# Performance work log

Measured on AMD Instinct MI355X. Metric: run time of the kernel, lower is better.

The kernel has to match this reference:

```python
import jax, jax.numpy as jnp
import numpy as np

B, T, D, H, L, F = 256, 32, 1024, 8, 3, 2048
SSRC, NCOL, NTAB, NACT, NSYM = 64, 32, 16, 64, 32
HD = D // H


def setup_inputs() -> dict:
    key = jax.random.key(0)
    ks = jax.random.split(key, 40)
    n = lambda k, s, sc=0.02: jax.random.normal(k, s, jnp.float32) * sc
    inp = {}
    inp["prev_action_emb"] = jax.random.normal(ks[0], (B, T, D), jnp.float32)
    inp["encoded_src"] = jax.random.normal(ks[1], (B, SSRC, D), jnp.float32)
    inp["encoded_col"] = jax.random.normal(ks[2], (B, NCOL, D), jnp.float32)
    inp["encoded_tab"] = jax.random.normal(ks[3], (B, NTAB, D), jnp.float32)
    inp["src_mask"] = jnp.zeros((B, SSRC), jnp.int32)  # 1 = padded
    inp["symbol_ids"] = jax.random.randint(ks[4], (B, T), 0, NSYM)
    inp["view_type"] = jax.random.randint(ks[5], (B,), 0, 3)  # 0=action,1=col,2=tab
    inp["gold_action"] = jax.random.randint(ks[6], (B,), 0, NACT)
    inp["gold_col"] = jax.random.randint(ks[7], (B,), 0, NCOL)
    inp["gold_tab"] = jax.random.randint(ks[8], (B,), 0, NTAB)
    # grammar embeddings (torch nn.Embedding default ~ N(0,1))
    inp["symbol_emb"] = jax.random.normal(ks[9], (NSYM, D), jnp.float32)
    inp["action_emb"] = jax.random.normal(ks[10], (NACT, D), jnp.float32)
    # affine heads
    inp["action_aff_w"] = n(ks[11], (D, D)); inp["action_aff_b"] = jnp.zeros((D,), jnp.float32)
    inp["symbol_aff_w"] = n(ks[12], (D, D)); inp["symbol_aff_b"] = jnp.zeros((D,), jnp.float32)
    inp["col_aff_w"] = n(ks[13], (D, D)); inp["col_aff_b"] = jnp.zeros((D,), jnp.float32)
    inp["tab_aff_w"] = n(ks[14], (D, D)); inp["tab_aff_b"] = jnp.zeros((D,), jnp.float32)
    inp["tgt_lin_w"] = n(ks[15], (2 * D, D)); inp["tgt_lin_b"] = jnp.zeros((D,), jnp.float32)
    inp["out_lin_w"] = n(ks[16], (D, D)); inp["out_lin_b"] = jnp.zeros((D,), jnp.float32)
    # transformer decoder layers (q,k,v,o stacked on axis 1)
    inp["self_w"] = n(ks[17], (L, 4, D, D)); inp["self_b"] = jnp.zeros((L, 4, D), jnp.float32)
    inp["cross_w"] = n(ks[18], (L, 4, D, D)); inp["cross_b"] = jnp.zeros((L, 4, D), jnp.float32)
    inp["ffn_w1"] = n(ks[19], (L, D, F)); inp["ffn_b1"] = jnp.zeros((L, F), jnp.float32)
    inp["ffn_w2"] = n(ks[20], (L, F, D)); inp["ffn_b2"] = jnp.zeros((L, D), jnp.float32)
    inp["ln_g"] = jnp.ones((L, 3, D), jnp.float32); inp["ln_b"] = jnp.zeros((L, 3, D), jnp.float32)
    return inp


def _pe(t, d):
    pos = jnp.arange(t, dtype=jnp.float32)[:, None]
    div = jnp.exp(jnp.arange(0, d, 2, dtype=jnp.float32) * (-np.log(10000.0) / d))
    pe = jnp.zeros((t, d), jnp.float32)
    pe = pe.at[:, 0::2].set(jnp.sin(pos * div)).at[:, 1::2].set(jnp.cos(pos * div))
    return pe


def _ln(x, g, b, eps=1e-5):
    m = jnp.mean(x, -1, keepdims=True)
    v = jnp.mean((x - m) ** 2, -1, keepdims=True)
    return (x - m) / jnp.sqrt(v + eps) * g + b


def _mha(xq, xkv, w, b, pad=None):
    # w: [4, D, D] for q,k,v,o; pad: [B, Tk] bool key-padding mask
    q = (xq @ w[0] + b[0]).reshape(xq.shape[0], -1, H, HD)
    k = (xkv @ w[1] + b[1]).reshape(xkv.shape[0], -1, H, HD)
    v = (xkv @ w[2] + b[2]).reshape(xkv.shape[0], -1, H, HD)
    s = jnp.einsum("bqhd,bkhd->bhqk", q, k) / np.sqrt(HD).astype(np.float32)
    if pad is not None:
        s = jnp.where(pad[:, None, None, :], -1e9, s)
    a = jax.nn.softmax(s, -1)
    o = jnp.einsum("bhqk,bkhd->bqhd", a, v).reshape(xq.shape[0], -1, D)
    return o @ w[3] + b[3]


def reference(prev_action_emb, encoded_src, encoded_col, encoded_tab, symbol_emb, action_emb,
              action_aff_w, action_aff_b, symbol_aff_w, symbol_aff_b, col_aff_w, col_aff_b,
              tab_aff_w, tab_aff_b, tgt_lin_w, tgt_lin_b, out_lin_w, out_lin_b,
              self_w, self_b, cross_w, cross_b, ffn_w1, ffn_b1, ffn_w2, ffn_b2, ln_g, ln_b,
              src_mask, symbol_ids, view_type, gold_action, gold_col, gold_tab):
    # target embeddings: affine(prev action emb) ++ affine(symbol emb gather)
    tgt_a = prev_action_emb @ action_aff_w + action_aff_b            # [B,T,D]
    tgt_s = symbol_emb[symbol_ids] @ symbol_aff_w + symbol_aff_b     # [B,T,D]
    x = jnp.concatenate([tgt_a, tgt_s], -1) @ tgt_lin_w + tgt_lin_b  # [B,T,D]
    x = x + _pe(T, D)[None]  # positional encoding (dropout = eval identity)
    pad = src_mask.astype(bool)
    for l in range(L):  # post-LN TransformerDecoderLayer (torch default, relu FFN)
        x = _ln(x + _mha(x, x, self_w[l], self_b[l]), ln_g[l, 0], ln_b[l, 0])
        x = _ln(x + _mha(x, encoded_src, cross_w[l], cross_b[l], pad), ln_g[l, 1], ln_b[l, 1])
        ff = jax.nn.relu(x @ ffn_w1[l] + ffn_b1[l]) @ ffn_w2[l] + ffn_b2[l]
        x = _ln(x + ff, ln_g[l, 2], ln_b[l, 2])
    out = x[:, -1, :] @ out_lin_w + out_lin_b  # [B,D], last decode position
    # three routed prediction heads: affine(src) . out -> masked log_softmax
    src_a = action_emb @ action_aff_w + action_aff_b                 # [A,D]
    logp_a = jax.nn.log_softmax(out @ src_a.T, -1)                   # [B,A]
    src_c = encoded_col @ col_aff_w + col_aff_b                      # [B,Nc,D]
    logp_c = jax.nn.log_softmax(jnp.einsum("bnd,bd->bn", src_c, out), -1)
    src_t = encoded_tab @ tab_aff_w + tab_aff_b                      # [B,Nt,D]
    logp_t = jax.nn.log_softmax(jnp.einsum("bnd,bd->bn", src_t, out), -1)
    ga = jnp.take_along_axis(logp_a, gold_action[:, None], 1)[:, 0]
    gc = jnp.take_along_axis(logp_c, gold_col[:, None], 1)[:, 0]
    gt = jnp.take_along_axis(logp_t, gold_tab[:, None], 1)[:, 0]
    # grammar routing: each example's loss comes from exactly one view
    nll = -jnp.where(view_type == 0, ga, jnp.where(view_type == 1, gc, gt))  # [B]
    return nll
```

## Files before the change

### kernel.cpp

```cpp
#include <hip/hip_runtime.h>

typedef float  f32x4 __attribute__((ext_vector_type(4)));
typedef short  s16x8 __attribute__((ext_vector_type(8)));

__device__ __forceinline__ float b2f(short s) {
    return __uint_as_float(((unsigned)(unsigned short)s) << 16);
}
__device__ __forceinline__ short f2b(float f) {
    unsigned u = __float_as_uint(f);
    u = u + 0x7fffu + ((u >> 16) & 1u);
    return (short)(u >> 16);
}

__device__ __forceinline__ void gld_lds16(const short* g, short* l) {
    __builtin_amdgcn_global_load_lds(
        (const __attribute__((address_space(1))) unsigned int*)(const void*)g,
        (__attribute__((address_space(3))) unsigned int*)(void*)l,
        16, 0, 0);
}

#define S_VMCNT0    asm volatile("s_waitcnt vmcnt(0)" ::: "memory")
#define S_LGKM0     asm volatile("s_waitcnt lgkmcnt(0)" ::: "memory")
#define SBAR        __builtin_amdgcn_s_barrier()
#define SCHED0      __builtin_amdgcn_sched_barrier(0)

template<int BM>
__global__ __launch_bounds__(512) void gemm_pipe(
    const short* __restrict__ A, const short* __restrict__ Bt,
    const float* __restrict__ bias,
    short* __restrict__ Cb,
    const short* __restrict__ res,
    const float* __restrict__ sym2, const int* __restrict__ sid,
    const float* __restrict__ pe,
    int M, int N, int K, int epi)
{
    constexpr int MF   = BM / 32;
    constexpr int ALW  = BM / 64;
    constexpr int BUFB = (BM + 256) * 128;
    __shared__ short lds[2 * (BM + 256) * 64];

    const int tid  = threadIdx.x;
    const int lane = tid & 63;
    const int wave = tid >> 6;

    int bid = blockIdx.x;
    int nwg = gridDim.x;
    if ((nwg & 7) == 0) { int q = nwg >> 3; bid = (bid & 7) * q + (bid >> 3); }
    const int nbx = N >> 8;
    const int m0 = (bid / nbx) * BM;
    const int n0 = (bid % nbx) * 256;

    const int wm = (wave >> 2) * (BM / 2);
    const int wn = (wave & 3) * 64;
    const int l15 = lane & 15, l4 = lane >> 4;
    const int key = lane & 7;

    f32x4 acc[MF][4];
#pragma unroll
    for (int m = 0; m < MF; m++)
#pragma unroll
        for (int n = 0; n < 4; n++)
#pragma unroll
            for (int j = 0; j < 4; j++) acc[m][n][j] = 0.f;

    int aoff[MF], boff[4];
#pragma unroll
    for (int m = 0; m < MF; m++) {
        int r = wm + m * 16 + l15;
        aoff[m] = r * 128 + ((l4 ^ key) << 4);
    }
#pragma unroll
    for (int n = 0; n < 4; n++) {
        int r = wn + n * 16 + l15;
        boff[n] = BM * 128 + r * 128 + ((l4 ^ key) << 4);
    }

    const int lrow = lane >> 3;
    const int lchunk = (lane & 7) ^ lrow;
    size_t agoff[ALW]; int aldo[ALW];
#pragma unroll
    for (int i = 0; i < ALW; i++) {
        int rr = wave * (BM / 8) + i * 8;
        agoff[i] = (size_t)(m0 + rr + lrow) * K + lchunk * 8;
        aldo[i]  = rr * 128;
    }
    size_t bgoff[4]; int bldo[4];
#pragma unroll
    for (int i = 0; i < 4; i++) {
        int rr = wave * 32 + i * 8;
        bgoff[i] = (size_t)(n0 + rr + lrow) * K + lchunk * 8;
        bldo[i]  = BM * 128 + rr * 128;
    }

    char* lbase = (char*)lds;
    auto stage = [&](int kt, int bufoff) {
        char* lb = lbase + bufoff;
        const size_t ke = (size_t)kt * 64;
#pragma unroll
        for (int i = 0; i < ALW; i++)
            gld_lds16(A + agoff[i] + ke, (short*)(lb + aldo[i]));
#pragma unroll
        for (int i = 0; i < 4; i++)
            gld_lds16(Bt + bgoff[i] + ke, (short*)(lb + bldo[i]));
    };

    const int NT = K >> 6;
    stage(0, 0);
    S_VMCNT0; SCHED0; SBAR; SCHED0;

    int cb = 0;
    for (int t = 0; t < NT; t++) {
        if (t + 1 < NT) stage(t + 1, (cb ^ 1) * BUFB);
        const char* cp = lbase + cb * BUFB;
        {
            s16x8 af[MF], bv[4];
#pragma unroll
            for (int m = 0; m < MF; m++) af[m] = *(const s16x8*)(cp + aoff[m]);
#pragma unroll
            for (int n = 0; n < 4; n++)  bv[n] = *(const s16x8*)(cp + boff[n]);
            S_LGKM0; SCHED0;
            __builtin_amdgcn_s_setprio(1);
#pragma unroll
            for (int m = 0; m < MF; m++)
#pragma unroll
                for (int n = 0; n < 4; n++)
                    acc[m][n] = __builtin_amdgcn_mfma_f32_16x16x32_bf16(
                        af[m], bv[n], acc[m][n], 0, 0, 0);
            __builtin_amdgcn_s_setprio(0);
        }
        {
            s16x8 af[MF], bv[4];
#pragma unroll
            for (int m = 0; m < MF; m++) af[m] = *(const s16x8*)(cp + (aoff[m] ^ 64));
#pragma unroll
            for (int n = 0; n < 4; n++)  bv[n] = *(const s16x8*)(cp + (boff[n] ^ 64));
            S_LGKM0; SCHED0;
            __builtin_amdgcn_s_setprio(1);
#pragma unroll
            for (int m = 0; m < MF; m++)
#pragma unroll
                for (int n = 0; n < 4; n++)
                    acc[m][n] = __builtin_amdgcn_mfma_f32_16x16x32_bf16(
                        af[m], bv[n], acc[m][n], 0, 0, 0);
            __builtin_amdgcn_s_setprio(0);
        }
        S_VMCNT0; SCHED0; SBAR; SCHED0;
        cb ^= 1;
    }

#pragma unroll
    for (int m = 0; m < MF; m++) {
#pragma unroll
        for (int n = 0; n < 4; n++) {
#pragma unroll
            for (int j = 0; j < 4; j++) {
                int row = m0 + wm + m * 16 + l4 * 4 + j;
                int col = n0 + wn + n * 16 + l15;
                float v = acc[m][n][j];
                if (bias) v += bias[col];
                size_t idx = (size_t)row * N + col;
                if (epi == 0) {
                    Cb[idx] = f2b(v);
                } else if (epi == 2) {
                    v += sym2[(size_t)sid[row] * 1024 + col] + pe[(size_t)(row & 31) * 1024 + col];
                    Cb[idx] = f2b(v);
                } else if (epi == 3) {
                    Cb[idx] = f2b(fmaxf(v, 0.f));
                } else {
                    Cb[idx] = f2b(v + b2f(res[idx]));
                }
            }
        }
    }
}

__global__ __launch_bounds__(256) void gemm_bt(
    const short* __restrict__ A, const short* __restrict__ Bt,
    const float* __restrict__ bias,
    float* __restrict__ Cf, short* __restrict__ Cb,
    const short* __restrict__ res,
    int M, int N, int K, int epi)
{
    __shared__ short As[128 * 64];
    __shared__ short Bs[128 * 64];
    const int tid  = threadIdx.x;
    const int lane = tid & 63;
    const int wave = tid >> 6;
    const int m0 = blockIdx.y * 128, n0 = blockIdx.x * 128;
    const int wm = (wave >> 1) * 64, wn = (wave & 1) * 64;
    const int l15 = lane & 15, l4 = lane >> 4;

    f32x4 acc[4][4];
#pragma unroll
    for (int m = 0; m < 4; m++)
#pragma unroll
        for (int n = 0; n < 4; n++)
#pragma unroll
            for (int j = 0; j < 4; j++) acc[m][n][j] = 0.f;

    const int srow = wave * 32 + (lane >> 3);
    const int scol = (lane & 7) * 8;
    const short* Ag = A  + (size_t)(m0 + srow) * K + scol;
    const short* Bg = Bt + (size_t)(n0 + srow) * K + scol;
    short* Al = As + (wave * 32) * 64;
    short* Bl = Bs + (wave * 32) * 64;

    for (int k0 = 0; k0 < K; k0 += 64) {
#pragma unroll
        for (int i = 0; i < 4; i++) {
            gld_lds16(Ag + (size_t)(i * 8) * K + k0, Al + i * 8 * 64);
            gld_lds16(Bg + (size_t)(i * 8) * K + k0, Bl + i * 8 * 64);
        }
        __syncthreads();
#pragma unroll
        for (int kk = 0; kk < 64; kk += 32) {
            s16x8 af[4], bfv[4];
#pragma unroll
            for (int m = 0; m < 4; m++)
                af[m] = *(const s16x8*)(As + (wm + m * 16 + l15) * 64 + kk + l4 * 8);
#pragma unroll
            for (int n = 0; n < 4; n++)
                bfv[n] = *(const s16x8*)(Bs + (wn + n * 16 + l15) * 64 + kk + l4 * 8);
#pragma unroll
            for (int m = 0; m < 4; m++)
#pragma unroll
                for (int n = 0; n < 4; n++)
                    acc[m][n] = __builtin_amdgcn_mfma_f32_16x16x32_bf16(
                        af[m], bfv[n], acc[m][n], 0, 0, 0);
        }
        __syncthreads();
    }

#pragma unroll
    for (int m = 0; m < 4; m++) {
#pragma unroll
        for (int n = 0; n < 4; n++) {
#pragma unroll
            for (int j = 0; j < 4; j++) {
                int row = m0 + wm + m * 16 + l4 * 4 + j;
                int col = n0 + wn + n * 16 + l15;
                float v = acc[m][n][j];
                if (bias) v += bias[col];
                size_t idx = (size_t)row * N + col;
                if (epi == 0) {
                    Cb[idx] = f2b(v);
                } else if (epi == 1) {
                    Cf[idx] = v;
                } else if (epi == 3) {
                    Cb[idx] = f2b(fmaxf(v, 0.f));
                } else if (epi == 6) {
                    Cb[idx] = f2b(v + b2f(res[idx]));
                } else {
                    Cf[idx] = v; Cb[idx] = f2b(v);
                }
            }
        }
    }
}

__global__ __launch_bounds__(256) void vecmat_bias(const float* __restrict__ Ab,
                                                   const float* __restrict__ Wt,
                                                   const float* __restrict__ tb,
                                                   float* __restrict__ out)
{
    int j = blockIdx.x * 256 + threadIdx.x;
    float s = tb[j];
    for (int k = 0; k < 1024; k++) s += Ab[k] * Wt[(size_t)k * 1024 + j];
    out[j] = s;
}

__global__ __launch_bounds__(256) void attn_self(const short* __restrict__ qkv,
                                                 short* __restrict__ o)
{
    const int b = blockIdx.x >> 3, h = blockIdx.x & 7;
    __shared__ short Q[32 * 128], Kk[32 * 128], Vv[32 * 128];
    __shared__ float S[32 * 32];
    const int tid = threadIdx.x;
    const size_t base = (size_t)b * 32 * 3072 + h * 128;
    for (int i = tid; i < 512; i += 256) {
        int r = i >> 4, c = (i & 15) * 8;
        size_t g = base + (size_t)r * 3072 + c;
        *(s16x8*)(Q  + r * 128 + c) = *(const s16x8*)(qkv + g);
        *(s16x8*)(Kk + r * 128 + c) = *(const s16x8*)(qkv + g + 1024);
        *(s16x8*)(Vv + r * 128 + c) = *(const s16x8*)(qkv + g + 2048);
    }
    __syncthreads();
    for (int i = tid; i < 1024; i += 256) {
        int r = i >> 5, c = i & 31;
        float s = 0.f;
        for (int d8 = 0; d8 < 16; d8++) {
            s16x8 qa = *(const s16x8*)(Q  + r * 128 + d8 * 8);
            s16x8 ka = *(const s16x8*)(Kk + c * 128 + d8 * 8);
#pragma unroll
            for (int j = 0; j < 8; j++) s += b2f(qa[j]) * b2f(ka[j]);
        }
        S[i] = s * 0.088388347648318447f;
    }
    __syncthreads();
    if (tid < 32) {
        float4* row = (float4*)(S + tid * 32);
        float mx = -1e30f;
#pragma unroll
        for (int c = 0; c < 8; c++) {
            float4 v4 = row[c];
            mx = fmaxf(mx, fmaxf(fmaxf(v4.x, v4.y), fmaxf(v4.z, v4.w)));
        }
        float sum = 0.f;
#pragma unroll
        for (int c = 0; c < 8; c++) {
            float4 v4 = row[c];
            v4.x = __expf(v4.x - mx); v4.y = __expf(v4.y - mx);
            v4.z = __expf(v4.z - mx); v4.w = __expf(v4.w - mx);
            sum += v4.x + v4.y + v4.z + v4.w;
            row[c] = v4;
        }
        float inv = 1.f / sum;
#pragma unroll
        for (int c = 0; c < 8; c++) {
            float4 v4 = row[c];
            v4.x *= inv; v4.y *= inv; v4.z *= inv; v4.w *= inv;
            row[c] = v4;
        }
    }
    __syncthreads();
    for (int g = tid; g < 512; g += 256) {
        int r = g >> 4, d0 = (g & 15) * 8;
        float a8[8] = {0.f,0.f,0.f,0.f,0.f,0.f,0.f,0.f};
        for (int c = 0; c < 32; c++) {
            float p = S[r * 32 + c];
            s16x8 v = *(const s16x8*)(Vv + c * 128 + d0);
#pragma unroll
            for (int j = 0; j < 8; j++) a8[j] += p * b2f(v[j]);
        }
        s16x8 ov;
#pragma unroll
        for (int j = 0; j < 8; j++) ov[j] = f2b(a8[j]);
        *(s16x8*)(o + (size_t)(b * 32 + r) * 1024 + h * 128 + d0) = ov;
    }
}

__global__ __launch_bounds__(256) void attn_cross(const short* __restrict__ q_,
                                                  const short* __restrict__ ckv,
                                                  const int* __restrict__ mask,
                                                  short* __restrict__ o)
{
    const int b = blockIdx.x >> 3, h = blockIdx.x & 7;
    __shared__ short Q[32 * 128], Kk[64 * 128], Vv[64 * 128];
    __shared__ float S[32 * 64];
    const int tid = threadIdx.x;
    for (int i = tid; i < 512; i += 256) {
        int r = i >> 4, c = (i & 15) * 8;
        *(s16x8*)(Q + r * 128 + c) = *(const s16x8*)(q_ + (size_t)(b * 32 + r) * 1024 + h * 128 + c);
    }
    for (int i = tid; i < 1024; i += 256) {
        int r = i >> 4, c = (i & 15) * 8;
        size_t g = (size_t)(b * 64 + r) * 2048 + h * 128 + c;
        *(s16x8*)(Kk + r * 128 + c) = *(const s16x8*)(ckv + g);
        *(s16x8*)(Vv + r * 128 + c) = *(const s16x8*)(ckv + g + 1024);
    }
    __syncthreads();
    for (int i = tid; i < 2048; i += 256) {
        int r = i >> 6, c = i & 63;
        float s = 0.f;
        for (int d8 = 0; d8 < 16; d8++) {
            s16x8 qa = *(const s16x8*)(Q  + r * 128 + d8 * 8);
            s16x8 ka = *(const s16x8*)(Kk + c * 128 + d8 * 8);
#pragma unroll
            for (int j = 0; j < 8; j++) s += b2f(qa[j]) * b2f(ka[j]);
        }
        s *= 0.088388347648318447f;
        if (mask[b * 64 + c] != 0) s = -1e9f;
        S[i] = s;
    }
    __syncthreads();
    if (tid < 32) {
        float4* row = (float4*)(S + tid * 64);
        float mx = -1e30f;
#pragma unroll
        for (int c = 0; c < 16; c++) {
            float4 v4 = row[c];
            mx = fmaxf(mx, fmaxf(fmaxf(v4.x, v4.y), fmaxf(v4.z, v4.w)));
        }
        float sum = 0.f;
#pragma unroll
        for (int c = 0; c < 16; c++) {
            float4 v4 = row[c];
            v4.x = __expf(v4.x - mx); v4.y = __expf(v4.y - mx);
            v4.z = __expf(v4.z - mx); v4.w = __expf(v4.w - mx);
            sum += v4.x + v4.y + v4.z + v4.w;
            row[c] = v4;
        }
        float inv = 1.f / sum;
#pragma unroll
        for (int c = 0; c < 16; c++) {
            float4 v4 = row[c];
            v4.x *= inv; v4.y *= inv; v4.z *= inv; v4.w *= inv;
            row[c] = v4;
        }
    }
    __syncthreads();
    for (int g = tid; g < 512; g += 256) {
        int r = g >> 4, d0 = (g & 15) * 8;
        float a8[8] = {0.f,0.f,0.f,0.f,0.f,0.f,0.f,0.f};
        for (int c = 0; c < 64; c++) {
            float p = S[r * 64 + c];
            s16x8 v = *(const s16x8*)(Vv + c * 128 + d0);
#pragma unroll
            for (int j = 0; j < 8; j++) a8[j] += p * b2f(v[j]);
        }
        s16x8 ov;
#pragma unroll
        for (int j = 0; j < 8; j++) ov[j] = f2b(a8[j]);
        *(s16x8*)(o + (size_t)(b * 32 + r) * 1024 + h * 128 + d0) = ov;
    }
}

__global__ __launch_bounds__(256) void attn_self_last(const short* __restrict__ q,
                                                      const short* __restrict__ kv,
                                                      short* __restrict__ out)
{
    __shared__ float qs[4][128];
    __shared__ float ps[4][32];
    const int wave = threadIdx.x >> 6, lane = threadIdx.x & 63;
    const int idx = blockIdx.x * 4 + wave;
    const int b = idx >> 3, h = idx & 7;
    for (int d = lane; d < 128; d += 64)
        qs[wave][d] = b2f(q[(size_t)b * 1024 + h * 128 + d]);
    __syncthreads();
    float s = -1e30f;
    if (lane < 32) {
        const short* kr = kv + (size_t)(b * 32 + lane) * 2048 + h * 128;
        float a = 0.f;
        for (int d = 0; d < 128; d += 8) {
            s16x8 kvv = *(const s16x8*)(kr + d);
#pragma unroll
            for (int j = 0; j < 8; j++) a += qs[wave][d + j] * b2f(kvv[j]);
        }
        s = a * 0.088388347648318447f;
    }
    float mx = s;
#pragma unroll
    for (int o = 1; o < 32; o <<= 1) mx = fmaxf(mx, __shfl_xor(mx, o));
    float p = (lane < 32) ? __expf(s - mx) : 0.f;
    float sum = p;
#pragma unroll
    for (int o = 1; o < 32; o <<= 1) sum += __shfl_xor(sum, o);
    if (lane < 32) ps[wave][lane] = p / sum;
    __syncthreads();
    for (int d = lane; d < 128; d += 64) {
        float a = 0.f;
        for (int j = 0; j < 32; j++)
            a += ps[wave][j] * b2f(kv[(size_t)(b * 32 + j) * 2048 + 1024 + h * 128 + d]);
        out[(size_t)b * 1024 + h * 128 + d] = f2b(a);
    }
}

__global__ __launch_bounds__(256) void attn_cross_last(const short* __restrict__ q,
                                                       const short* __restrict__ ckv,
                                                       const int* __restrict__ mask,
                                                       short* __restrict__ out)
{
    __shared__ float qs[4][128];
    __shared__ float ps[4][64];
    const int wave = threadIdx.x >> 6, lane = threadIdx.x & 63;
    const int idx = blockIdx.x * 4 + wave;
    const int b = idx >> 3, h = idx & 7;
    for (int d = lane; d < 128; d += 64)
        qs[wave][d] = b2f(q[(size_t)b * 1024 + h * 128 + d]);
    __syncthreads();
    const short* kr = ckv + (size_t)(b * 64 + lane) * 2048 + h * 128;
    float a = 0.f;
    for (int d = 0; d < 128; d += 8) {
        s16x8 kvv = *(const s16x8*)(kr + d);
#pragma unroll
        for (int j = 0; j < 8; j++) a += qs[wave][d + j] * b2f(kvv[j]);
    }
    float s = a * 0.088388347648318447f;
    if (mask[b * 64 + lane] != 0) s = -1e9f;
    float mx = s;
#pragma unroll
    for (int o = 1; o < 64; o <<= 1) mx = fmaxf(mx, __shfl_xor(mx, o));
    float p = __expf(s - mx);
    float sum = p;
#pragma unroll
    for (int o = 1; o < 64; o <<= 1) sum += __shfl_xor(sum, o);
    ps[wave][lane] = p / sum;
    __syncthreads();
    for (int d = lane; d < 128; d += 64) {
        float acc = 0.f;
        for (int j = 0; j < 64; j++)
            acc += ps[wave][j] * b2f(ckv[(size_t)(b * 64 + j) * 2048 + 1024 + h * 128 + d]);
        out[(size_t)b * 1024 + h * 128 + d] = f2b(acc);
    }
}

__global__ __launch_bounds__(128) void ln_rows_b(const short* __restrict__ X,
                                                 short* __restrict__ Y,
                                                 const float* __restrict__ g,
                                                 const float* __restrict__ bt)
{
    const int row = blockIdx.x, tid = threadIdx.x;
    s16x8 v = *(const s16x8*)(X + (size_t)row * 1024 + tid * 8);
    float f[8];
    float s = 0.f, q = 0.f;
#pragma unroll
    for (int j = 0; j < 8; j++) { f[j] = b2f(v[j]); s += f[j]; q += f[j] * f[j]; }
#pragma unroll
    for (int o = 1; o < 64; o <<= 1) { s += __shfl_xor(s, o); q += __shfl_xor(q, o); }
    __shared__ float ls[2], lq[2];
    if ((tid & 63) == 0) { ls[tid >> 6] = s; lq[tid >> 6] = q; }
    __syncthreads();
    s = ls[0] + ls[1];
    q = lq[0] + lq[1];
    const float mean = s * 0.0009765625f;
    const float var  = q * 0.0009765625f - mean * mean;
    const float rs = rsqrtf(var + 1e-5f);
    s16x8 ov;
#pragma unroll
    for (int j = 0; j < 8; j++) {
        int c = tid * 8 + j;
        ov[j] = f2b((f[j] - mean) * rs * g[c] + bt[c]);
    }
    *(s16x8*)(Y + (size_t)row * 1024 + tid * 8) = ov;
}

__global__ __launch_bounds__(256) void convf2b(const float* __restrict__ s,
                                               short* __restrict__ d, int n)
{
    int i = (blockIdx.x * 256 + threadIdx.x) * 8;
    if (i < n) {
        float4 a = *(const float4*)(s + i);
        float4 b = *(const float4*)(s + i + 4);
        s16x8 o;
        o[0] = f2b(a.x); o[1] = f2b(a.y); o[2] = f2b(a.z); o[3] = f2b(a.w);
        o[4] = f2b(b.x); o[5] = f2b(b.y); o[6] = f2b(b.z); o[7] = f2b(b.w);
        *(s16x8*)(d + i) = o;
    }
}

__global__ __launch_bounds__(256) void transpose_conv_b(const float* __restrict__ src0,
                                                        short* __restrict__ dst0,
                                                        int R, int C)
{
    const float* src = src0 + (size_t)blockIdx.z * R * C;
    short* dst = dst0 + (size_t)blockIdx.z * R * C;
    __shared__ float t[32][33];
    int c0 = blockIdx.x * 32, r0 = blockIdx.y * 32;
    int tx = threadIdx.x & 31, ty = threadIdx.x >> 5;
#pragma unroll
    for (int i = 0; i < 32; i += 8) t[ty + i][tx] = src[(size_t)(r0 + ty + i) * C + c0 + tx];
    __syncthreads();
#pragma unroll
    for (int i = 0; i < 32; i += 8) dst[(size_t)(c0 + ty + i) * R + r0 + tx] = f2b(t[tx][ty + i]);
}

__global__ __launch_bounds__(256) void pad_conv(const float* __restrict__ s,
                                                short* __restrict__ d, int src_rows)
{
    int i = blockIdx.x * 256 + threadIdx.x;
    int r = i >> 10;
    d[i] = (r < src_rows) ? f2b(s[i]) : (short)0;
}

__global__ __launch_bounds__(256) void pe_build(float* __restrict__ pe)
{
    int i = blockIdx.x * 256 + threadIdx.x;
    int t = i >> 10, d = i & 1023;
    int de = d & ~1;
    float ang = (float)t * expf((float)de * (-9.2103403719761836f / 1024.f));
    pe[i] = (d & 1) ? cosf(ang) : sinf(ang);
}

__global__ __launch_bounds__(256) void gather_last(const short* __restrict__ x,
                                                   short* __restrict__ xlast)
{
    int i = blockIdx.x * 256 + threadIdx.x;
    int b = i >> 10, d = i & 1023;
    xlast[i] = x[((size_t)(b * 32 + 31) << 10) + d];
}

__global__ __launch_bounds__(64) void head_final(
    const float* __restrict__ logits_a,
    const float* __restrict__ enc_col_f, const short* __restrict__ yc,
    const float* __restrict__ enc_tab_f, const short* __restrict__ yt,
    const float* __restrict__ outf,
    const float* __restrict__ col_b, const float* __restrict__ tab_b,
    const int* __restrict__ view, const int* __restrict__ ga,
    const int* __restrict__ gc, const int* __restrict__ gt,
    float* __restrict__ nll)
{
    const int b = blockIdx.x, lane = threadIdx.x;
    const int vt = view[b];
    if (vt == 0) {
        float x = logits_a[(size_t)b * 128 + lane];
        float mx = x;
#pragma unroll
        for (int o = 1; o < 64; o <<= 1) mx = fmaxf(mx, __shfl_xor(mx, o));
        float sum = __expf(x - mx);
#pragma unroll
        for (int o = 1; o < 64; o <<= 1) sum += __shfl_xor(sum, o);
        float lse = mx + logf(sum);
        float gl = __shfl(x, ga[b]);
        if (lane == 0) nll[b] = lse - gl;
    } else {
        const int nit = (vt == 1) ? 32 : 16;
        const float* enc = (vt == 1) ? (enc_col_f + (size_t)b * 32 * 1024)
                                     : (enc_tab_f + (size_t)b * 16 * 1024);
        const short* y   = (vt == 1) ? (yc + (size_t)b * 1024) : (yt + (size_t)b * 1024);
        const float* bb  = (vt == 1) ? col_b : tab_b;
        float bc = 0.f;
        for (int i = lane; i < 1024; i += 64) bc += bb[i] * outf[(size_t)b * 1024 + i];
#pragma unroll
        for (int o = 1; o < 64; o <<= 1) bc += __shfl_xor(bc, o);
        float logit = -1e30f;
        if (lane < nit) {
            float s = bc;
            const float* er = enc + (size_t)lane * 1024;
            for (int d8 = 0; d8 < 128; d8++) {
                s16x8 yv = *(const s16x8*)(y + d8 * 8);
                float4 e0 = *(const float4*)(er + d8 * 8);
                float4 e1 = *(const float4*)(er + d8 * 8 + 4);
                s += e0.x * b2f(yv[0]) + e0.y * b2f(yv[1]) + e0.z * b2f(yv[2]) + e0.w * b2f(yv[3])
                   + e1.x * b2f(yv[4]) + e1.y * b2f(yv[5]) + e1.z * b2f(yv[6]) + e1.w * b2f(yv[7]);
            }
            logit = s;
        }
        float mx = logit;
#pragma unroll
        for (int o = 1; o < 64; o <<= 1) mx = fmaxf(mx, __shfl_xor(mx, o));
        float sum = (lane < nit) ? __expf(logit - mx) : 0.f;
#pragma unroll
        for (int o = 1; o < 64; o <<= 1) sum += __shfl_xor(sum, o);
        float lse = mx + logf(sum);
        int g = (vt == 1) ? gc[b] : gt[b];
        float gl = __shfl(logit, g);
        if (lane == 0) nll[b] = lse - gl;
    }
}

extern "C" void kernel_launch(void* const* d_in, const int* in_sizes, int n_in,
                              void* d_out, int out_size, void* d_ws, size_t ws_size,
                              hipStream_t stream)
{
    const float* pa_f     = (const float*)d_in[0];
    const float* src_f    = (const float*)d_in[1];
    const float* colenc_f = (const float*)d_in[2];
    const float* tabenc_f = (const float*)d_in[3];
    const int*   src_mask = (const int*)d_in[4];
    const int*   sym_ids  = (const int*)d_in[5];
    const int*   view     = (const int*)d_in[6];
    const int*   gold_a   = (const int*)d_in[7];
    const int*   gold_c   = (const int*)d_in[8];
    const int*   gold_t   = (const int*)d_in[9];
    const float* sym_emb  = (const float*)d_in[10];
    const float* act_emb  = (const float*)d_in[11];
    const float* Aaff_w   = (const float*)d_in[12];
    const float* Aaff_b   = (const float*)d_in[13];
    const float* Saff_w   = (const float*)d_in[14];
    const float* Saff_b   = (const float*)d_in[15];
    const float* Caff_w   = (const float*)d_in[16];
    const float* Caff_b   = (const float*)d_in[17];
    const float* Taff_w   = (const float*)d_in[18];
    const float* Taff_b   = (const float*)d_in[19];
    const float* tgt_w    = (const float*)d_in[20];
    const float* tgt_b    = (const float*)d_in[21];
    const float* outw     = (const float*)d_in[22];
    const float* outbias  = (const float*)d_in[23];
    const float* self_w   = (const float*)d_in[24];
    const float* self_b   = (const float*)d_in[25];
    const float* cross_w  = (const float*)d_in[26];
    const float* cross_b  = (const float*)d_in[27];
    const float* f1w      = (const float*)d_in[28];
    const float* f1b      = (const float*)d_in[29];
    const float* f2w      = (const float*)d_in[30];
    const float* f2bb     = (const float*)d_in[31];
    const float* lng      = (const float*)d_in[32];
    const float* lnbt     = (const float*)d_in[33];
    float* nll = (float*)d_out;

    char* ws = (char*)d_ws;
    size_t off = 0;
    auto alloc = [&](size_t bytes) -> char* {
        off = (off + 255) & ~(size_t)255;
        char* p = ws + off; off += bytes; return p;
    };

    const size_t MB1 = (size_t)1024 * 1024;
    short* WAaff  = (short*)alloc(MB1 * 2);
    short* WSaff  = (short*)alloc(MB1 * 2);
    short* Wtop   = (short*)alloc(MB1 * 2);
    short* Wbot   = (short*)alloc(MB1 * 2);
    short* Wout   = (short*)alloc(MB1 * 2);
    short* Wcol   = (short*)alloc(MB1 * 2);
    short* Wtab   = (short*)alloc(MB1 * 2);
    short* Aaffrm = (short*)alloc(MB1 * 2);
    short* Wcomb  = (short*)alloc(MB1 * 2);
    float* cbias  = (float*)alloc(1024 * 4);
    short* Wself  = (short*)alloc(12 * MB1 * 2);
    short* Wcross = (short*)alloc(12 * MB1 * 2);
    short* Wf1a   = (short*)alloc(3 * 2 * MB1 * 2);
    short* Wf2a   = (short*)alloc(3 * 2 * MB1 * 2);

    short* src_bf   = (short*)alloc((size_t)16384 * 1024 * 2);
    short* sym_pad  = (short*)alloc((size_t)128 * 1024 * 2);
    short* act_pad  = (short*)alloc((size_t)128 * 1024 * 2);
    short* sa_out   = (short*)alloc((size_t)128 * 1024 * 2);
    float* sym2     = (float*)alloc((size_t)128 * 1024 * 4);
    float* pe       = (float*)alloc((size_t)32 * 1024 * 4);
    short* attn     = (short*)alloc((size_t)8192 * 1024 * 2);
    short* x_bf     = (short*)alloc((size_t)8192 * 1024 * 2);
    short* tmpb     = (short*)alloc((size_t)8192 * 1024 * 2);
    short* arena    = (short*)alloc((size_t)16384 * 2048 * 2);
    short* xlast    = (short*)alloc((size_t)256 * 1024 * 2);
    float* outf     = (float*)alloc((size_t)256 * 1024 * 4);
    short* outb16   = (short*)alloc((size_t)256 * 1024 * 2);
    short* srca     = (short*)alloc((size_t)128 * 1024 * 2);
    float* logits_a = (float*)alloc((size_t)256 * 128 * 4);
    short* ycb      = (short*)alloc((size_t)256 * 1024 * 2);
    short* ytb      = (short*)alloc((size_t)256 * 1024 * 2);
    short* xq31     = (short*)alloc((size_t)256 * 1024 * 2);
    short* x256a    = (short*)alloc((size_t)256 * 1024 * 2);
    short* x256b    = (short*)alloc((size_t)256 * 1024 * 2);
    short* q256     = (short*)alloc((size_t)256 * 1024 * 2);
    short* cq256    = (short*)alloc((size_t)256 * 1024 * 2);
    short* o256     = (short*)alloc((size_t)256 * 1024 * 2);
    short* h256     = (short*)alloc((size_t)256 * 2048 * 2);
    short* tmpb256  = (short*)alloc((size_t)256 * 1024 * 2);

    short* pa_bf = tmpb;
    short* cq    = tmpb;

    const dim3 BLK(256);
    auto conv = [&](const float* s, short* d, size_t n) {
        convf2b<<<dim3((unsigned)(n / 8 / 256)), BLK, 0, stream>>>(s, d, (int)n);
    };
    auto trans = [&](const float* s, short* d, int R, int C, int nm) {
        transpose_conv_b<<<dim3(C / 32, R / 32, nm), BLK, 0, stream>>>(s, d, R, C);
    };
    auto gp = [&](const short* A, const short* Bt, const float* bias,
                  short* Cb, const short* res,
                  const float* sy, const int* si, const float* pp,
                  int M, int N, int K, int epi, int BM) {
        if (BM == 256)
            gemm_pipe<256><<<dim3((N / 256) * (M / 256)), dim3(512), 0, stream>>>(
                A, Bt, bias, Cb, res, sy, si, pp, M, N, K, epi);
        else
            gemm_pipe<128><<<dim3((N / 256) * (M / 128)), dim3(512), 0, stream>>>(
                A, Bt, bias, Cb, res, sy, si, pp, M, N, K, epi);
    };
    auto gsm = [&](const short* A, const short* Bt, const float* bias,
                   float* Cf, short* Cb, const short* res,
                   int M, int N, int K, int epi) {
        gemm_bt<<<dim3(N / 128, M / 128), BLK, 0, stream>>>(
            A, Bt, bias, Cf, Cb, res, M, N, K, epi);
    };

    pe_build<<<dim3(128), BLK, 0, stream>>>(pe);
    conv(pa_f, pa_bf, (size_t)8192 * 1024);
    conv(src_f, src_bf, (size_t)16384 * 1024);
    conv(Caff_w, Wcol, MB1);
    conv(Taff_w, Wtab, MB1);
    conv(Aaff_w, Aaffrm, MB1);
    pad_conv<<<dim3(512), BLK, 0, stream>>>(sym_emb, sym_pad, 32);
    pad_conv<<<dim3(512), BLK, 0, stream>>>(act_emb, act_pad, 64);
    trans(Aaff_w, WAaff, 1024, 1024, 1);
    trans(Saff_w, WSaff, 1024, 1024, 1);
    trans(tgt_w, Wtop, 1024, 1024, 1);
    trans(tgt_w + MB1, Wbot, 1024, 1024, 1);
    trans(outw, Wout, 1024, 1024, 1);
    trans(self_w, Wself, 1024, 1024, 12);
    trans(cross_w, Wcross, 1024, 1024, 12);
    trans(f1w, Wf1a, 1024, 2048, 3);
    trans(f2w, Wf2a, 2048, 1024, 3);

    gsm(Wtop, Aaffrm, nullptr, nullptr, Wcomb, nullptr, 1024, 1024, 1024, 0);
    vecmat_bias<<<dim3(4), BLK, 0, stream>>>(Aaff_b, tgt_w, tgt_b, cbias);
    gsm(sym_pad, WSaff, Saff_b, nullptr, sa_out, nullptr, 128, 1024, 1024, 0);
    gsm(sa_out, Wbot, nullptr, sym2, nullptr, nullptr, 128, 1024, 1024, 1);
    gp(pa_bf, Wcomb, cbias, x_bf, nullptr, sym2, sym_ids, pe,
       8192, 1024, 1024, 2, 128);

    for (int l = 0; l < 2; l++) {
        const float* sb = self_b + (size_t)l * 4096;
        const float* cb = cross_b + (size_t)l * 4096;
        gp(x_bf, Wself + (size_t)(4 * l) * MB1, sb, arena, nullptr, nullptr, nullptr, nullptr,
           8192, 3072, 1024, 0, 256);
        attn_self<<<dim3(2048), BLK, 0, stream>>>(arena, attn);
        gp(attn, Wself + (size_t)(4 * l + 3) * MB1, sb + 3072, tmpb, x_bf, nullptr, nullptr, nullptr,
           8192, 1024, 1024, 6, 128);
        ln_rows_b<<<dim3(8192), dim3(128), 0, stream>>>(tmpb, x_bf,
            lng + (size_t)(l * 3 + 0) * 1024, lnbt + (size_t)(l * 3 + 0) * 1024);
        gp(x_bf, Wcross + (size_t)(4 * l) * MB1, cb, cq, nullptr, nullptr, nullptr, nullptr,
           8192, 1024, 1024, 0, 128);
        gp(src_bf, Wcross + (size_t)(4 * l + 1) * MB1, cb + 1024, arena, nullptr, nullptr, nullptr, nullptr,
           16384, 2048, 1024, 0, 256);
        attn_cross<<<dim3(2048), BLK, 0, stream>>>(cq, arena, src_mask, attn);
        gp(attn, Wcross + (size_t)(4 * l + 3) * MB1, cb + 3072, tmpb, x_bf, nullptr, nullptr, nullptr,
           8192, 1024, 1024, 6, 128);
        ln_rows_b<<<dim3(8192), dim3(128), 0, stream>>>(tmpb, x_bf,
            lng + (size_t)(l * 3 + 1) * 1024, lnbt + (size_t)(l * 3 + 1) * 1024);
        gp(x_bf, Wf1a + (size_t)l * 2 * MB1, f1b + (size_t)l * 2048, arena, nullptr, nullptr, nullptr, nullptr,
           8192, 2048, 1024, 3, 256);
        gp(arena, Wf2a + (size_t)l * 2 * MB1, f2bb + (size_t)l * 1024, tmpb, x_bf, nullptr, nullptr, nullptr,
           8192, 1024, 2048, 6, 128);
        ln_rows_b<<<dim3(8192), dim3(128), 0, stream>>>(tmpb, x_bf,
            lng + (size_t)(l * 3 + 2) * 1024, lnbt + (size_t)(l * 3 + 2) * 1024);
    }

    {
        const float* sb = self_b + (size_t)2 * 4096;
        const float* cb = cross_b + (size_t)2 * 4096;
        gather_last<<<dim3(1024), BLK, 0, stream>>>(x_bf, xq31);
        gp(x_bf, Wself + (size_t)(4 * 2 + 1) * MB1, sb + 1024, arena, nullptr, nullptr, nullptr, nullptr,
           8192, 2048, 1024, 0, 256);
        gsm(xq31, Wself + (size_t)(4 * 2) * MB1, sb, nullptr, q256, nullptr, 256, 1024, 1024, 0);
        attn_self_last<<<dim3(512), BLK, 0, stream>>>(q256, arena, o256);
        gsm(o256, Wself + (size_t)(4 * 2 + 3) * MB1, sb + 3072, nullptr, tmpb256, xq31, 256, 1024, 1024, 6);
        ln_rows_b<<<dim3(256), dim3(128), 0, stream>>>(tmpb256, x256a,
            lng + (size_t)(2 * 3 + 0) * 1024, lnbt + (size_t)(2 * 3 + 0) * 1024);
        gsm(x256a, Wcross + (size_t)(4 * 2) * MB1, cb, nullptr, cq256, nullptr, 256, 1024, 1024, 0);
        gp(src_bf, Wcross + (size_t)(4 * 2 + 1) * MB1, cb + 1024, arena, nullptr, nullptr, nullptr, nullptr,
           16384, 2048, 1024, 0, 256);
        attn_cross_last<<<dim3(512), BLK, 0, stream>>>(cq256, arena, src_mask, o256);
        gsm(o256, Wcross + (size_t)(4 * 2 + 3) * MB1, cb + 3072, nullptr, tmpb256, x256a, 256, 1024, 1024, 6);
        ln_rows_b<<<dim3(256), dim3(128), 0, stream>>>(tmpb256, x256b,
            lng + (size_t)(2 * 3 + 1) * 1024, lnbt + (size_t)(2 * 3 + 1) * 1024);
        gsm(x256b, Wf1a + (size_t)2 * 2 * MB1, f1b + (size_t)2 * 2048, nullptr, h256, nullptr,
            256, 2048, 1024, 3);
        gsm(h256, Wf2a + (size_t)2 * 2 * MB1, f2bb + (size_t)2 * 1024, nullptr, tmpb256, x256b,
            256, 1024, 2048, 6);
        ln_rows_b<<<dim3(256), dim3(128), 0, stream>>>(tmpb256, xlast,
            lng + (size_t)(2 * 3 + 2) * 1024, lnbt + (size_t)(2 * 3 + 2) * 1024);
    }

    gsm(xlast, Wout, outbias, outf, outb16, nullptr, 256, 1024, 1024, 5);
    gsm(act_pad, WAaff, Aaff_b, nullptr, srca, nullptr, 128, 1024, 1024, 0);
    gsm(outb16, srca, nullptr, logits_a, nullptr, nullptr, 256, 128, 1024, 1);
    gsm(outb16, Wcol, nullptr, nullptr, ycb, nullptr, 256, 1024, 1024, 0);
    gsm(outb16, Wtab, nullptr, nullptr, ytb, nullptr, 256, 1024, 1024, 0);
    head_final<<<dim3(256), dim3(64), 0, stream>>>(
        logits_a, colenc_f, ycb, tabenc_f, ytb, outf,
        Caff_b, Taff_b, view, gold_a, gold_c, gold_t, nll);
}
```

Baseline: 2.535 ms.

## Replace double-buffered large-tile GEMM with small-tile single-buffer high-occupancy GEMM

Swaps the 512-thread, 128/256x256-tile, double-buffered LDS pipeline GEMM for a 256-thread 64x128-tile kernel with a single LDS buffer and plain __syncthreads, launched with bounds of 4 blocks per CU. All large decoder GEMMs now use this kernel. The intent is to hide latency through occupancy and more workgroups rather than explicit prefetch. The trade is lower data reuse per tile, more global traffic, and no overlap of loads with MFMA inside a block.

```diff
diff --git a/kernel.cpp b/kernel.cpp
--- a/kernel.cpp
+++ b/kernel.cpp
@@ -19,13 +19,7 @@
         16, 0, 0);
 }
 
-#define S_VMCNT0    asm volatile("s_waitcnt vmcnt(0)" ::: "memory")
-#define S_LGKM0     asm volatile("s_waitcnt lgkmcnt(0)" ::: "memory")
-#define SBAR        __builtin_amdgcn_s_barrier()
-#define SCHED0      __builtin_amdgcn_sched_barrier(0)
-
-template<int BM>
-__global__ __launch_bounds__(512) void gemm_pipe(
+__global__ __launch_bounds__(256, 4) void gemm_hi(
     const short* __restrict__ A, const short* __restrict__ Bt,
     const float* __restrict__ bias,
     short* __restrict__ Cb,
@@ -34,122 +28,92 @@
     const float* __restrict__ pe,
     int M, int N, int K, int epi)
 {
-    constexpr int MF   = BM / 32;
-    constexpr int ALW  = BM / 64;
-    constexpr int BUFB = (BM + 256) * 128;
-    __shared__ short lds[2 * (BM + 256) * 64];
+    __shared__ short lds[(64 + 128) * 64];
 
     const int tid  = threadIdx.x;
     const int lane = tid & 63;
-    const int wave = tid >> 6;
+    const int w    = tid >> 6;
 
     int bid = blockIdx.x;
     int nwg = gridDim.x;
     if ((nwg & 7) == 0) { int q = nwg >> 3; bid = (bid & 7) * q + (bid >> 3); }
-    const int nbx = N >> 8;
-    const int m0 = (bid / nbx) * BM;
-    const int n0 = (bid % nbx) * 256;
-
-    const int wm = (wave >> 2) * (BM / 2);
-    const int wn = (wave & 3) * 64;
+    const int nbx = N >> 7;
+    const int m0 = (bid / nbx) * 64;
+    const int n0 = (bid % nbx) * 128;
+
+    const int wm = (w >> 1) * 32;
+    const int wn = (w & 1) * 64;
     const int l15 = lane & 15, l4 = lane >> 4;
     const int key = lane & 7;
 
-    f32x4 acc[MF][4];
-#pragma unroll
-    for (int m = 0; m < MF; m++)
+    f32x4 acc[2][4];
+#pragma unroll
+    for (int m = 0; m < 2; m++)
 #pragma unroll
         for (int n = 0; n < 4; n++)
 #pragma unroll
             for (int j = 0; j < 4; j++) acc[m][n][j] = 0.f;
 
-    int aoff[MF], boff[4];
-#pragma unroll
-    for (int m = 0; m < MF; m++) {
+    int aoff[2], boff[4];
+#pragma unroll
+    for (int m = 0; m < 2; m++) {
         int r = wm + m * 16 + l15;
         aoff[m] = r * 128 + ((l4 ^ key) << 4);
     }
 #pragma unroll
     for (int n = 0; n < 4; n++) {
         int r = wn + n * 16 + l15;
-        boff[n] = BM * 128 + r * 128 + ((l4 ^ key) << 4);
+        boff[n] = 64 * 128 + r * 128 + ((l4 ^ key) << 4);
     }
 
     const int lrow = lane >> 3;
     const int lchunk = (lane & 7) ^ lrow;
-    size_t agoff[ALW]; int aldo[ALW];
-#pragma unroll
-    for (int i = 0; i < ALW; i++) {
-        int rr = wave * (BM / 8) + i * 8;
+    size_t agoff[2]; int aldo[2];
+#pragma unroll
+    for (int i = 0; i < 2; i++) {
+        int rr = w * 16 + i * 8;
         agoff[i] = (size_t)(m0 + rr + lrow) * K + lchunk * 8;
         aldo[i]  = rr * 128;
     }
     size_t bgoff[4]; int bldo[4];
 #pragma unroll
     for (int i = 0; i < 4; i++) {
-        int rr = wave * 32 + i * 8;
+        int rr = w * 32 + i * 8;
         bgoff[i] = (size_t)(n0 + rr + lrow) * K + lchunk * 8;
-        bldo[i]  = BM * 128 + rr * 128;
-    }
-
-    char* lbase = (char*)lds;
-    auto stage = [&](int kt, int bufoff) {
-        char* lb = lbase + bufoff;
-        const size_t ke = (size_t)kt * 64;
-#pragma unroll
-        for (int i = 0; i < ALW; i++)
+        bldo[i]  = 64 * 128 + rr * 128;
+    }
+
+    char* lb = (char*)lds;
+    const int NT = K >> 6;
+    for (int t = 0; t < NT; t++) {
+        const size_t ke = (size_t)t * 64;
+#pragma unroll
+        for (int i = 0; i < 2; i++)
             gld_lds16(A + agoff[i] + ke, (short*)(lb + aldo[i]));
 #pragma unroll
         for (int i = 0; i < 4; i++)
             gld_lds16(Bt + bgoff[i] + ke, (short*)(lb + bldo[i]));
-    };
-
-    const int NT = K >> 6;
-    stage(0, 0);
-    S_VMCNT0; SCHED0; SBAR; SCHED0;
-
-    int cb = 0;
-    for (int t = 0; t < NT; t++) {
-        if (t + 1 < NT) stage(t + 1, (cb ^ 1) * BUFB);
-        const char* cp = lbase + cb * BUFB;
-        {
-            s16x8 af[MF], bv[4];
-#pragma unroll
-            for (int m = 0; m < MF; m++) af[m] = *(const s16x8*)(cp + aoff[m]);
-#pragma unroll
-            for (int n = 0; n < 4; n++)  bv[n] = *(const s16x8*)(cp + boff[n]);
-            S_LGKM0; SCHED0;
-            __builtin_amdgcn_s_setprio(1);
-#pragma unroll
-            for (int m = 0; m < MF; m++)
+        __syncthreads();
+#pragma unroll
+        for (int ks = 0; ks < 2; ks++) {
+            const int x = ks ? 64 : 0;
+            s16x8 af[2], bv[4];
+#pragma unroll
+            for (int m = 0; m < 2; m++) af[m] = *(const s16x8*)(lb + (aoff[m] ^ x));
+#pragma unroll
+            for (int n = 0; n < 4; n++)  bv[n] = *(const s16x8*)(lb + (boff[n] ^ x));
+#pragma unroll
+            for (int m = 0; m < 2; m++)
 #pragma unroll
                 for (int n = 0; n < 4; n++)
                     acc[m][n] = __builtin_amdgcn_mfma_f32_16x16x32_bf16(
                         af[m], bv[n], acc[m][n], 0, 0, 0);
-            __builtin_amdgcn_s_setprio(0);
-        }
-        {
-            s16x8 af[MF], bv[4];
-#pragma unroll
-            for (int m = 0; m < MF; m++) af[m] = *(const s16x8*)(cp + (aoff[m] ^ 64));
-#pragma unroll
-            for (int n = 0; n < 4; n++)  bv[n] = *(const s16x8*)(cp + (boff[n] ^ 64));
-            S_LGKM0; SCHED0;
-            __builtin_amdgcn_s_setprio(1);
-#pragma unroll
-            for (int m = 0; m < MF; m++)
-#pragma unroll
-                for (int n = 0; n < 4; n++)
-                    acc[m][n] = __builtin_amdgcn_mfma_f32_16x16x32_bf16(
-                        af[m], bv[n], acc[m][n], 0, 0, 0);
-            __builtin_amdgcn_s_setprio(0);
-        }
-        S_VMCNT0; SCHED0; SBAR; SCHED0;
-        cb ^= 1;
-    }
-
-#pragma unroll
-    for (int m = 0; m < MF; m++) {
+        }
+        __syncthreads();
+    }
+
+#pragma unroll
+    for (int m = 0; m < 2; m++) {
 #pragma unroll
         for (int n = 0; n < 4; n++) {
 #pragma unroll
@@ -737,16 +701,12 @@
     auto trans = [&](const float* s, short* d, int R, int C, int nm) {
         transpose_conv_b<<<dim3(C / 32, R / 32, nm), BLK, 0, stream>>>(s, d, R, C);
     };
-    auto gp = [&](const short* A, const short* Bt, const float* bias,
+    auto gh = [&](const short* A, const short* Bt, const float* bias,
                   short* Cb, const short* res,
                   const float* sy, const int* si, const float* pp,
-                  int M, int N, int K, int epi, int BM) {
-        if (BM == 256)
-            gemm_pipe<256><<<dim3((N / 256) * (M / 256)), dim3(512), 0, stream>>>(
-                A, Bt, bias, Cb, res, sy, si, pp, M, N, K, epi);
-        else
-            gemm_pipe<128><<<dim3((N / 256) * (M / 128)), dim3(512), 0, stream>>>(
-                A, Bt, bias, Cb, res, sy, si, pp, M, N, K, epi);
+                  int M, int N, int K, int epi) {
+        gemm_hi<<<dim3((N / 128) * (M / 64)), BLK, 0, stream>>>(
+            A, Bt, bias, Cb, res, sy, si, pp, M, N, K, epi);
     };
     auto gsm = [&](const short* A, const short* Bt, const float* bias,
                    float* Cf, short* Cb, const short* res,
@@ -777,32 +737,32 @@
     vecmat_bias<<<dim3(4), BLK, 0, stream>>>(Aaff_b, tgt_w, tgt_b, cbias);
     gsm(sym_pad, WSaff, Saff_b, nullptr, sa_out, nullptr, 128, 1024, 1024, 0);
     gsm(sa_out, Wbot, nullptr, sym2, nullptr, nullptr, 128, 1024, 1024, 1);
-    gp(pa_bf, Wcomb, cbias, x_bf, nullptr, sym2, sym_ids, pe,
-       8192, 1024, 1024, 2, 128);
+    gh(pa_bf, Wcomb, cbias, x_bf, nullptr, sym2, sym_ids, pe,
+       8192, 1024, 1024, 2);
 
     for (int l = 0; l < 2; l++) {
         const float* sb = self_b + (size_t)l * 4096;
         const float* cb = cross_b + (size_t)l * 4096;
-        gp(x_bf, Wself + (size_t)(4 * l) * MB1, sb, arena, nullptr, nullptr, nullptr, nullptr,
-           8192, 3072, 1024, 0, 256);
+        gh(x_bf, Wself + (size_t)(4 * l) * MB1, sb, arena, nullptr, nullptr, nullptr, nullptr,
+           8192, 3072, 1024, 0);
         attn_self<<<dim3(2048), BLK, 0, stream>>>(arena, attn);
-        gp(attn, Wself + (size_t)(4 * l + 3) * MB1, sb + 3072, tmpb, x_bf, nullptr, nullptr, nullptr,
-           8192, 1024, 1024, 6, 128);
+        gh(attn, Wself + (size_t)(4 * l + 3) * MB1, sb + 3072, tmpb, x_bf, nullptr, nullptr, nullptr,
+           8192, 1024, 1024, 6);
         ln_rows_b<<<dim3(8192), dim3(128), 0, stream>>>(tmpb, x_bf,
             lng + (size_t)(l * 3 + 0) * 1024, lnbt + (size_t)(l * 3 + 0) * 1024);
-        gp(x_bf, Wcross + (size_t)(4 * l) * MB1, cb, cq, nullptr, nullptr, nullptr, nullptr,
-           8192, 1024, 1024, 0, 128);
-        gp(src_bf, Wcross + (size_t)(4 * l + 1) * MB1, cb + 1024, arena, nullptr, nullptr, nullptr, nullptr,
-           16384, 2048, 1024, 0, 256);
+        gh(x_bf, Wcross + (size_t)(4 * l) * MB1, cb, cq, nullptr, nullptr, nullptr, nullptr,
+           8192, 1024, 1024, 0);
+        gh(src_bf, Wcross + (size_t)(4 * l + 1) * MB1, cb + 1024, arena, nullptr, nullptr, nullptr, nullptr,
+           16384, 2048, 1024, 0);
         attn_cross<<<dim3(2048), BLK, 0, stream>>>(cq, arena, src_mask, attn);
-        gp(attn, Wcross + (size_t)(4 * l + 3) * MB1, cb + 3072, tmpb, x_bf, nullptr, nullptr, nullptr,
-           8192, 1024, 1024, 6, 128);
+        gh(attn, Wcross + (size_t)(4 * l + 3) * MB1, cb + 3072, tmpb, x_bf, nullptr, nullptr, nullptr,
+           8192, 1024, 1024, 6);
         ln_rows_b<<<dim3(8192), dim3(128), 0, stream>>>(tmpb, x_bf,
             lng + (size_t)(l * 3 + 1) * 1024, lnbt + (size_t)(l * 3 + 1) * 1024);
-        gp(x_bf, Wf1a + (size_t)l * 2 * MB1, f1b + (size_t)l * 2048, arena, nullptr, nullptr, nullptr, nullptr,
-           8192, 2048, 1024, 3, 256);
-        gp(arena, Wf2a + (size_t)l * 2 * MB1, f2bb + (size_t)l * 1024, tmpb, x_bf, nullptr, nullptr, nullptr,
-           8192, 1024, 2048, 6, 128);
+        gh(x_bf, Wf1a + (size_t)l * 2 * MB1, f1b + (size_t)l * 2048, arena, nullptr, nullptr, nullptr, nullptr,
+           8192, 2048, 1024, 3);
+        gh(arena, Wf2a + (size_t)l * 2 * MB1, f2bb + (size_t)l * 1024, tmpb, x_bf, nullptr, nullptr, nullptr,
+           8192, 1024, 2048, 6);
         ln_rows_b<<<dim3(8192), dim3(128), 0, stream>>>(tmpb, x_bf,
             lng + (size_t)(l * 3 + 2) * 1024, lnbt + (size_t)(l * 3 + 2) * 1024);
     }
@@ -811,16 +771,16 @@
         const float* sb = self_b + (size_t)2 * 4096;
         const float* cb = cross_b + (size_t)2 * 4096;
         gather_last<<<dim3(1024), BLK, 0, stream>>>(x_bf, xq31);
-        gp(x_bf, Wself + (size_t)(4 * 2 + 1) * MB1, sb + 1024, arena, nullptr, nullptr, nullptr, nullptr,
-           8192, 2048, 1024, 0, 256);
+        gh(x_bf, Wself + (size_t)(4 * 2 + 1) * MB1, sb + 1024, arena, nullptr, nullptr, nullptr, nullptr,
+           8192, 2048, 1024, 0);
         gsm(xq31, Wself + (size_t)(4 * 2) * MB1, sb, nullptr, q256, nullptr, 256, 1024, 1024, 0);
         attn_self_last<<<dim3(512), BLK, 0, stream>>>(q256, arena, o256);
         gsm(o256, Wself + (size_t)(4 * 2 + 3) * MB1, sb + 3072, nullptr, tmpb256, xq31, 256, 1024, 1024, 6);
         ln_rows_b<<<dim3(256), dim3(128), 0, stream>>>(tmpb256, x256a,
             lng + (size_t)(2 * 3 + 0) * 1024, lnbt + (size_t)(2 * 3 + 0) * 1024);
         gsm(x256a, Wcross + (size_t)(4 * 2) * MB1, cb, nullptr, cq256, nullptr, 256, 1024, 1024, 0);
-        gp(src_bf, Wcross + (size_t)(4 * 2 + 1) * MB1, cb + 1024, arena, nullptr, nullptr, nullptr, nullptr,
-           16384, 2048, 1024, 0, 256);
+        gh(src_bf, Wcross + (size_t)(4 * 2 + 1) * MB1, cb + 1024, arena, nullptr, nullptr, nullptr, nullptr,
+           16384, 2048, 1024, 0);
         attn_cross_last<<<dim3(512), BLK, 0, stream>>>(cq256, arena, src_mask, o256);
         gsm(o256, Wcross + (size_t)(4 * 2 + 3) * MB1, cb + 3072, nullptr, tmpb256, x256a, 256, 1024, 1024, 6);
         ln_rows_b<<<dim3(256), dim3(128), 0, stream>>>(tmpb256, x256b,
```

Result: faster. 2.277 ms (-10.2%).
